# Kernel optimization log

Hardware: AMD Instinct MI355X
Metric: run time of the kernel (lower is better)

Reference implementation:

```python
import jax, jax.numpy as jnp
import numpy as np
from jax import lax

B, C, O, K, H, Wd = 8, 64, 64, 3, 128, 128


def setup_inputs() -> dict:
    key = jax.random.key(0)
    k1, k2, k3 = jax.random.split(key, 3)
    feat = jax.random.normal(k1, (B, C, H, Wd), dtype=jnp.float32)
    transform_mat = jax.random.normal(k2, (B, K * K, H * Wd), dtype=jnp.float32)
    # xavier-normal init for W [C, K, K, O]
    std = float(np.sqrt(2.0 / (C * K * K + O)))
    W = jax.random.normal(k3, (C, K, K, O), dtype=jnp.float32) * std
    return {"feat": feat, "transform_mat": transform_mat, "W": W}


def reference(feat, transform_mat, W):
    b, c, h, w = feat.shape
    L = h * w
    # unfold: [B, C*K*K, H, W] with channel-major (c, ki, kj) ordering, same as torch Unfold
    patches = lax.conv_general_dilated_patches(
        feat, filter_shape=(K, K), window_strides=(1, 1),
        padding=((1, 1), (1, 1)))
    p = patches.reshape(b, c, K * K, L)                 # [B, C, K*K, L]
    trans = jnp.transpose(transform_mat, (0, 2, 1))     # [B, L, K*K] (module's permute(0,2,1))
    Wr = W.reshape(c, K * K, -1)                        # [C, K*K, O]
    # dynamic weighted conv: per-location filter scales each patch tap before contraction
    out = jnp.einsum('bckl,blk,cko->bol', p, trans, Wr)  # [B, O, L]
    return out.reshape(b, -1, h, w)
```

## Files before the change

kernel.cpp:

```cpp
#include <hip/hip_runtime.h>

#define NTAP 9
#define C_DIM 64
#define O_DIM 64
#define HW 128
#define CPAD 72

typedef short s16x8 __attribute__((ext_vector_type(8)));
typedef float f32x16 __attribute__((ext_vector_type(16)));

__device__ __forceinline__ unsigned short f2bf(float x) {
    unsigned int u = __float_as_uint(x);
    unsigned int r = (u + 0x7fffu + ((u >> 16) & 1u)) >> 16;
    return (unsigned short)r;
}

__global__ void swizzle_W_kernel(const float* __restrict__ W,
                                 unsigned short* __restrict__ Wf) {
    int idx = blockIdx.x * 256 + threadIdx.x;
    if (idx >= NTAP * 4 * 2 * 64 * 8) return;
    int e    = idx & 7;
    int lane = (idx >> 3) & 63;
    int m    = (idx >> 9) & 1;
    int s    = (idx >> 10) & 3;
    int tap  = idx >> 12;
    int c = s * 16 + ((lane >> 5) << 3) + e;
    int o = (m << 5) + (lane & 31);
    Wf[idx] = f2bf(W[c * 576 + tap * 64 + o]);
}

__global__ __launch_bounds__(256, 4) void dyconv_kernel(
    const float* __restrict__ feat, const float* __restrict__ tm,
    const unsigned short* __restrict__ Wf, float* __restrict__ out)
{
    __shared__ __align__(16) unsigned short feat_lds[3][66][CPAD];

    const int flat  = blockIdx.x;
    const int b     = flat & 7;
    const int inner = flat >> 3;
    const int h     = inner >> 1;
    const int w0    = (inner & 1) << 6;

    const int tid = threadIdx.x;

    for (int U = tid; U < 432; U += 256) {
        const int q   = U % 18;
        const int ro  = U / 18;
        const int oct = ro & 7;
        const int r   = ro >> 3;
        const int hr  = h - 1 + r;
        const int wb  = w0 - 4 + 4 * q;
        const bool ld = (hr >= 0) && (hr < HW) && (wb >= 0) && (wb <= HW - 4);
        const float* src = feat + (((size_t)(b * C_DIM + oct * 8)) * HW + hr) * HW + wb;
        float4 v[8];
        #pragma unroll
        for (int j = 0; j < 8; ++j)
            v[j] = ld ? *(const float4*)(src + (size_t)j * (HW * HW))
                      : float4{0.f, 0.f, 0.f, 0.f};
        #pragma unroll
        for (int i = 0; i < 4; ++i) {
            const int wi = 4 * q - 3 + i;
            if (wi >= 0 && wi <= 65) {
                s16x8 pk;
                #pragma unroll
                for (int j = 0; j < 8; ++j) {
                    const float* vf = (const float*)&v[j];
                    pk[j] = (short)f2bf(vf[i]);
                }
                *(s16x8*)&feat_lds[r][wi][oct * 8] = pk;
            }
        }
    }

    const int lane = tid & 63;
    const int wave = tid >> 6;
    const int m    = wave >> 1;
    const int pg   = wave & 1;
    const int g    = lane >> 5;
    const int c31  = lane & 31;
    const int wout = w0 + pg * 32 + c31;

    float tmr[NTAP];
    #pragma unroll
    for (int t = 0; t < NTAP; ++t)
        tmr[t] = tm[((size_t)(b * NTAP + t)) * (HW * HW) + (size_t)h * HW + wout];

    __syncthreads();

    const s16x8* __restrict__ Wf8 = (const s16x8*)Wf;

    f32x16 acc = {0,0,0,0,0,0,0,0,0,0,0,0,0,0,0,0};

    __builtin_amdgcn_s_setprio(1);
    #pragma unroll
    for (int tap = 0; tap < NTAP; ++tap) {
        const int di = tap / 3;
        const int dj = tap % 3;
        const s16x8* bp = (const s16x8*)&feat_lds[di][pg * 32 + c31 + dj][0];
        f32x16 pa = {0,0,0,0,0,0,0,0,0,0,0,0,0,0,0,0};
        #pragma unroll
        for (int s = 0; s < 4; ++s) {
            s16x8 bf = bp[2 * s + g];
            s16x8 a  = Wf8[((tap * 4 + s) * 2 + m) * 64 + lane];
            pa = __builtin_amdgcn_mfma_f32_32x32x16_bf16(a, bf, pa, 0, 0, 0);
        }
        const float tv = tmr[tap];
        #pragma unroll
        for (int r = 0; r < 16; ++r)
            acc[r] = fmaf(tv, pa[r], acc[r]);
    }
    __builtin_amdgcn_s_setprio(0);

    float* op = out + ((size_t)b * O_DIM) * (HW * HW) + (size_t)h * HW + wout;
    #pragma unroll
    for (int r = 0; r < 16; ++r) {
        const int o = (r & 3) + ((r >> 2) << 3) + (g << 2) + (m << 5);
        op[(size_t)o * (HW * HW)] = acc[r];
    }
}

extern "C" void kernel_launch(void* const* d_in, const int* in_sizes, int n_in,
                              void* d_out, int out_size, void* d_ws, size_t ws_size,
                              hipStream_t stream) {
    const float* feat = (const float*)d_in[0];
    const float* tm   = (const float*)d_in[1];
    const float* W    = (const float*)d_in[2];
    float* out        = (float*)d_out;
    unsigned short* Wf = (unsigned short*)d_ws;

    swizzle_W_kernel<<<dim3(144), dim3(256), 0, stream>>>(W, Wf);
    dyconv_kernel<<<dim3(2048), dim3(256), 0, stream>>>(feat, tm, Wf, out);
}
```

Before: 31.13 us.

## Compute two output rows per block to reuse halo rows and W fragments

Each block now handles two adjacent output rows, staging 4 input rows in LDS instead of 3. This reduces redundant global feature loads from 3x to 2x, and each W fragment load feeds two MFMAs. The LDS channel slots are XOR-swizzled to cut bank conflicts on the strided reads. The grid halves to 1024 blocks, with more LDS and registers per block, which can lower occupancy.

```diff
diff --git a/kernel.cpp b/kernel.cpp
--- a/kernel.cpp
+++ b/kernel.cpp
@@ -33,89 +33,131 @@
     const float* __restrict__ feat, const float* __restrict__ tm,
     const unsigned short* __restrict__ Wf, float* __restrict__ out)
 {
-    __shared__ __align__(16) unsigned short feat_lds[3][66][CPAD];
+    __shared__ __align__(16) unsigned short feat_lds[4][66][CPAD];
 
     const int flat  = blockIdx.x;
     const int b     = flat & 7;
     const int inner = flat >> 3;
-    const int h     = inner >> 1;
+    const int h0    = (inner >> 1) * 2;
     const int w0    = (inner & 1) << 6;
 
-    const int tid = threadIdx.x;
-
-    for (int U = tid; U < 432; U += 256) {
-        const int q   = U % 18;
-        const int ro  = U / 18;
-        const int oct = ro & 7;
-        const int r   = ro >> 3;
-        const int hr  = h - 1 + r;
-        const int wb  = w0 - 4 + 4 * q;
-        const bool ld = (hr >= 0) && (hr < HW) && (wb >= 0) && (wb <= HW - 4);
-        const float* src = feat + (((size_t)(b * C_DIM + oct * 8)) * HW + hr) * HW + wb;
-        float4 v[8];
-        #pragma unroll
-        for (int j = 0; j < 8; ++j)
-            v[j] = ld ? *(const float4*)(src + (size_t)j * (HW * HW))
-                      : float4{0.f, 0.f, 0.f, 0.f};
-        #pragma unroll
-        for (int i = 0; i < 4; ++i) {
-            const int wi = 4 * q - 3 + i;
-            if (wi >= 0 && wi <= 65) {
-                s16x8 pk;
-                #pragma unroll
-                for (int j = 0; j < 8; ++j) {
-                    const float* vf = (const float*)&v[j];
-                    pk[j] = (short)f2bf(vf[i]);
-                }
-                *(s16x8*)&feat_lds[r][wi][oct * 8] = pk;
-            }
-        }
-    }
-
+    const int tid  = threadIdx.x;
     const int lane = tid & 63;
     const int wave = tid >> 6;
     const int m    = wave >> 1;
     const int pg   = wave & 1;
     const int g    = lane >> 5;
     const int c31  = lane & 31;
-    const int wout = w0 + pg * 32 + c31;
+    const int pw   = pg * 32 + c31;
+    const int wout = w0 + pw;
 
-    float tmr[NTAP];
+    float tmr0[NTAP], tmr1[NTAP];
     #pragma unroll
-    for (int t = 0; t < NTAP; ++t)
-        tmr[t] = tm[((size_t)(b * NTAP + t)) * (HW * HW) + (size_t)h * HW + wout];
+    for (int t = 0; t < NTAP; ++t) {
+        const float* tp = tm + ((size_t)(b * NTAP + t)) * (HW * HW)
+                        + (size_t)h0 * HW + wout;
+        tmr0[t] = tp[0];
+        tmr1[t] = tp[HW];
+    }
+
+    {
+        auto unit_addr = [&](int U, int& r, int& q, int& oct, const float*& src,
+                             bool& ld) {
+            oct = U & 7;
+            const int t6 = U >> 3;
+            q  = t6 % 18;
+            r  = t6 / 18;
+            const int hr = h0 - 1 + r;
+            const int wb = w0 - 4 + 4 * q;
+            ld = (hr >= 0) && (hr < HW) && (wb >= 0) && (wb <= HW - 4);
+            src = feat + (((size_t)(b * C_DIM + oct * 8)) * HW + hr) * HW + wb;
+        };
+        auto unit_store = [&](int r, int q, int oct, const float4* v) {
+            #pragma unroll
+            for (int i = 0; i < 4; ++i) {
+                const int wi = 4 * q - 3 + i;
+                if (wi >= 0 && wi <= 65) {
+                    const int slot = oct ^ ((wi >> 3) & 3);
+                    s16x8 pk;
+                    #pragma unroll
+                    for (int j = 0; j < 8; ++j) {
+                        const float* vf = (const float*)&v[j];
+                        pk[j] = (short)f2bf(vf[i]);
+                    }
+                    *(s16x8*)&feat_lds[r][wi][slot * 8] = pk;
+                }
+            }
+        };
+
+        int r0, q0, o0, r1, q1, o1;
+        bool ld0, ld1;
+        const float *s0, *s1;
+        unit_addr(tid,       r0, q0, o0, s0, ld0);
+        unit_addr(tid + 256, r1, q1, o1, s1, ld1);
+        float4 v0[8], v1[8];
+        #pragma unroll
+        for (int j = 0; j < 8; ++j)
+            v0[j] = ld0 ? *(const float4*)(s0 + (size_t)j * (HW * HW))
+                        : float4{0.f, 0.f, 0.f, 0.f};
+        #pragma unroll
+        for (int j = 0; j < 8; ++j)
+            v1[j] = ld1 ? *(const float4*)(s1 + (size_t)j * (HW * HW))
+                        : float4{0.f, 0.f, 0.f, 0.f};
+        unit_store(r0, q0, o0, v0);
+        unit_store(r1, q1, o1, v1);
+        if (tid < 576 - 512) {
+            int r2, q2, o2; bool ld2; const float* s2;
+            unit_addr(tid + 512, r2, q2, o2, s2, ld2);
+            float4 v2[8];
+            #pragma unroll
+            for (int j = 0; j < 8; ++j)
+                v2[j] = ld2 ? *(const float4*)(s2 + (size_t)j * (HW * HW))
+                            : float4{0.f, 0.f, 0.f, 0.f};
+            unit_store(r2, q2, o2, v2);
+        }
+    }
 
     __syncthreads();
 
     const s16x8* __restrict__ Wf8 = (const s16x8*)Wf;
 
-    f32x16 acc = {0,0,0,0,0,0,0,0,0,0,0,0,0,0,0,0};
+    f32x16 acc0 = {0,0,0,0,0,0,0,0,0,0,0,0,0,0,0,0};
+    f32x16 acc1 = acc0;
 
     __builtin_amdgcn_s_setprio(1);
     #pragma unroll
     for (int tap = 0; tap < NTAP; ++tap) {
         const int di = tap / 3;
         const int dj = tap % 3;
-        const s16x8* bp = (const s16x8*)&feat_lds[di][pg * 32 + c31 + dj][0];
-        f32x16 pa = {0,0,0,0,0,0,0,0,0,0,0,0,0,0,0,0};
+        const int wi = pw + dj;
+        const int cb = (wi >> 3) & 3;
+        f32x16 pa0 = {0,0,0,0,0,0,0,0,0,0,0,0,0,0,0,0};
+        f32x16 pa1 = pa0;
         #pragma unroll
         for (int s = 0; s < 4; ++s) {
-            s16x8 bf = bp[2 * s + g];
-            s16x8 a  = Wf8[((tap * 4 + s) * 2 + m) * 64 + lane];
-            pa = __builtin_amdgcn_mfma_f32_32x32x16_bf16(a, bf, pa, 0, 0, 0);
+            const int slot = (2 * s + g) ^ cb;
+            s16x8 bf0 = *(const s16x8*)&feat_lds[di    ][wi][slot * 8];
+            s16x8 bf1 = *(const s16x8*)&feat_lds[di + 1][wi][slot * 8];
+            s16x8 a   = Wf8[((tap * 4 + s) * 2 + m) * 64 + lane];
+            pa0 = __builtin_amdgcn_mfma_f32_32x32x16_bf16(a, bf0, pa0, 0, 0, 0);
+            pa1 = __builtin_amdgcn_mfma_f32_32x32x16_bf16(a, bf1, pa1, 0, 0, 0);
         }
-        const float tv = tmr[tap];
+        const float tv0 = tmr0[tap];
+        const float tv1 = tmr1[tap];
         #pragma unroll
-        for (int r = 0; r < 16; ++r)
-            acc[r] = fmaf(tv, pa[r], acc[r]);
+        for (int r = 0; r < 16; ++r) {
+            acc0[r] = fmaf(tv0, pa0[r], acc0[r]);
+            acc1[r] = fmaf(tv1, pa1[r], acc1[r]);
+        }
     }
     __builtin_amdgcn_s_setprio(0);
 
-    float* op = out + ((size_t)b * O_DIM) * (HW * HW) + (size_t)h * HW + wout;
+    float* op = out + ((size_t)b * O_DIM) * (HW * HW) + (size_t)h0 * HW + wout;
     #pragma unroll
     for (int r = 0; r < 16; ++r) {
         const int o = (r & 3) + ((r >> 2) << 3) + (g << 2) + (m << 5);
-        op[(size_t)o * (HW * HW)] = acc[r];
+        op[(size_t)o * (HW * HW)]      = acc0[r];
+        op[(size_t)o * (HW * HW) + HW] = acc1[r];
     }
 }
 
@@ -129,5 +171,5 @@
     unsigned short* Wf = (unsigned short*)d_ws;
 
     swizzle_W_kernel<<<dim3(144), dim3(256), 0, stream>>>(W, Wf);
-    dyconv_kernel<<<dim3(2048), dim3(256), 0, stream>>>(feat, tm, Wf, out);
+    dyconv_kernel<<<dim3(1024), dim3(256), 0, stream>>>(feat, tm, Wf, out);
 }
```

Result: slower. 48.56 us (+56.0%).

## Compute two output rows per block with XOR-swizzled LDS feature tile

Applied to the files above, without the earlier changes.

Each block now computes two adjacent output rows with 512 threads, loading a 4-row halo tile instead of 3 rows per single output row. This reduces redundant feature loads and bf16 conversion across neighbouring rows. The LDS padding is replaced by an XOR swizzle of channel-octet slots to avoid bank conflicts without the extra space. The load loop is restructured so consecutive threads cover channel octets. The grid is halved, which lowers block-level parallelism and raises per-block register and LDS pressure.

```diff
diff --git a/kernel.cpp b/kernel.cpp
--- a/kernel.cpp
+++ b/kernel.cpp
@@ -4,7 +4,6 @@
 #define C_DIM 64
 #define O_DIM 64
 #define HW 128
-#define CPAD 72
 
 typedef short s16x8 __attribute__((ext_vector_type(8)));
 typedef float f32x16 __attribute__((ext_vector_type(16)));
@@ -29,26 +28,36 @@
     Wf[idx] = f2bf(W[c * 576 + tap * 64 + o]);
 }
 
-__global__ __launch_bounds__(256, 4) void dyconv_kernel(
+__global__ __launch_bounds__(512, 4) void dyconv_kernel(
     const float* __restrict__ feat, const float* __restrict__ tm,
     const unsigned short* __restrict__ Wf, float* __restrict__ out)
 {
-    __shared__ __align__(16) unsigned short feat_lds[3][66][CPAD];
+    __shared__ __align__(16) unsigned short feat_lds[4][66][64];
 
     const int flat  = blockIdx.x;
     const int b     = flat & 7;
     const int inner = flat >> 3;
-    const int h     = inner >> 1;
+    const int h0    = (inner >> 1) * 2;
     const int w0    = (inner & 1) << 6;
 
-    const int tid = threadIdx.x;
+    const int tid  = threadIdx.x;
+    const int lane = tid & 63;
+    const int wave = tid >> 6;
+    const int hrow = (wave >> 2) & 1;
+    const int m    = (wave >> 1) & 1;
+    const int pg   = wave & 1;
+    const int g    = lane >> 5;
+    const int c31  = lane & 31;
+    const int pw   = pg * 32 + c31;
+    const int wout = w0 + pw;
+    const int hout = h0 + hrow;
 
-    for (int U = tid; U < 432; U += 256) {
-        const int q   = U % 18;
-        const int ro  = U / 18;
-        const int oct = ro & 7;
-        const int r   = ro >> 3;
-        const int hr  = h - 1 + r;
+    auto do_unit = [&](int U) {
+        const int oct = U & 7;
+        const int t6  = U >> 3;
+        const int q   = t6 % 18;
+        const int r   = t6 / 18;
+        const int hr  = h0 - 1 + r;
         const int wb  = w0 - 4 + 4 * q;
         const bool ld = (hr >= 0) && (hr < HW) && (wb >= 0) && (wb <= HW - 4);
         const float* src = feat + (((size_t)(b * C_DIM + oct * 8)) * HW + hr) * HW + wb;
@@ -61,29 +70,25 @@
         for (int i = 0; i < 4; ++i) {
             const int wi = 4 * q - 3 + i;
             if (wi >= 0 && wi <= 65) {
+                const int slot = oct ^ (wi & 7);
                 s16x8 pk;
                 #pragma unroll
                 for (int j = 0; j < 8; ++j) {
                     const float* vf = (const float*)&v[j];
                     pk[j] = (short)f2bf(vf[i]);
                 }
-                *(s16x8*)&feat_lds[r][wi][oct * 8] = pk;
+                *(s16x8*)&feat_lds[r][wi][slot * 8] = pk;
             }
         }
-    }
-
-    const int lane = tid & 63;
-    const int wave = tid >> 6;
-    const int m    = wave >> 1;
-    const int pg   = wave & 1;
-    const int g    = lane >> 5;
-    const int c31  = lane & 31;
-    const int wout = w0 + pg * 32 + c31;
+    };
 
     float tmr[NTAP];
     #pragma unroll
     for (int t = 0; t < NTAP; ++t)
-        tmr[t] = tm[((size_t)(b * NTAP + t)) * (HW * HW) + (size_t)h * HW + wout];
+        tmr[t] = tm[((size_t)(b * NTAP + t)) * (HW * HW) + (size_t)hout * HW + wout];
+
+    do_unit(tid);
+    if ((tid & 7) == 0) do_unit(512 + (tid >> 3));
 
     __syncthreads();
 
@@ -96,11 +101,13 @@
     for (int tap = 0; tap < NTAP; ++tap) {
         const int di = tap / 3;
         const int dj = tap % 3;
-        const s16x8* bp = (const s16x8*)&feat_lds[di][pg * 32 + c31 + dj][0];
+        const int wi = pw + dj;
+        const int sw = wi & 7;
         f32x16 pa = {0,0,0,0,0,0,0,0,0,0,0,0,0,0,0,0};
         #pragma unroll
         for (int s = 0; s < 4; ++s) {
-            s16x8 bf = bp[2 * s + g];
+            const int slot = (2 * s + g) ^ sw;
+            s16x8 bf = *(const s16x8*)&feat_lds[hrow + di][wi][slot * 8];
             s16x8 a  = Wf8[((tap * 4 + s) * 2 + m) * 64 + lane];
             pa = __builtin_amdgcn_mfma_f32_32x32x16_bf16(a, bf, pa, 0, 0, 0);
         }
@@ -111,7 +118,7 @@
     }
     __builtin_amdgcn_s_setprio(0);
 
-    float* op = out + ((size_t)b * O_DIM) * (HW * HW) + (size_t)h * HW + wout;
+    float* op = out + ((size_t)b * O_DIM) * (HW * HW) + (size_t)hout * HW + wout;
     #pragma unroll
     for (int r = 0; r < 16; ++r) {
         const int o = (r & 3) + ((r >> 2) << 3) + (g << 2) + (m << 5);
@@ -129,5 +136,5 @@
     unsigned short* Wf = (unsigned short*)d_ws;
 
     swizzle_W_kernel<<<dim3(144), dim3(256), 0, stream>>>(W, Wf);
-    dyconv_kernel<<<dim3(2048), dim3(256), 0, stream>>>(feat, tm, Wf, out);
+    dyconv_kernel<<<dim3(1024), dim3(512), 0, stream>>>(feat, tm, Wf, out);
 }
```

After: 38.49 us. 1.24x slower.
